# Kernel optimization log

Measured on AMD Instinct MI355X. Metric: run time of the kernel, lower is better.

## Reference

```python
import jax, jax.numpy as jnp
import numpy as np

C = 32            # multiplicity per irrep (node irreps = 32x0e + 32x1o)
N_NODES = 50000
N_EDGES = 800000
R_DIM = 8         # radial embedding dim
R_HID = 8         # radial MLP hidden width
N_SPECIES = 5
AVG_NEIGH = 16.0
N_PATHS = 4       # 0ex0e->0e, 0ex1o->1o, 1ox0e->1o, 1ox1o->0e


def setup_inputs() -> dict:
    key = jax.random.key(0)
    ks = jax.random.split(key, 16)
    inp = {
        'node_features': jax.random.normal(ks[0], (N_NODES, 4 * C), jnp.float32),
        'edge_features': jax.random.normal(ks[1], (N_EDGES, 4), jnp.float32),
        'radial_embedding': jax.random.normal(ks[2], (N_EDGES, R_DIM), jnp.float32),
        'senders': jax.random.randint(ks[3], (N_EDGES,), 0, N_NODES),
        'receivers': jax.random.randint(ks[4], (N_EDGES,), 0, N_NODES),
        'node_species': jax.random.randint(ks[5], (N_NODES,), 0, N_SPECIES),
        # linear_up: per-irrep (block-diagonal) mixing
        'W_up_s': jax.random.normal(ks[6], (C, C), jnp.float32),
        'W_up_v': jax.random.normal(ks[7], (C, C), jnp.float32),
        # radial MLP (no biases, e3nn-style): R_DIM -> R_HID -> N_PATHS*C
        'W_r1': jax.random.normal(ks[8], (R_DIM, R_HID), jnp.float32),
        'W_r2': jax.random.normal(ks[9], (R_HID, N_PATHS * C), jnp.float32),
        # linear_down: 2C x 0e -> 2C (C feats + C gates); 2C x 1o -> C x 1o
        'W_down_s': jax.random.normal(ks[10], (2 * C, 2 * C), jnp.float32),
        'W_down_v': jax.random.normal(ks[11], (2 * C, C), jnp.float32),
        # species-indexed skip connection to gate irreps
        'W_skip_s': jax.random.normal(ks[12], (N_SPECIES, C, 2 * C), jnp.float32),
        'W_skip_v': jax.random.normal(ks[13], (N_SPECIES, C, C), jnp.float32),
    }
    return inp


def reference(node_features, edge_features, radial_embedding, senders, receivers,
              node_species, W_up_s, W_up_v, W_r1, W_r2, W_down_s, W_down_v,
              W_skip_s, W_skip_v):
    N = node_features.shape[0]
    inv_sqrt_C = 1.0 / np.sqrt(C)
    # split irreps: scalars [N,C] and vectors [N,C,3]
    s = node_features[:, :C]
    v = node_features[:, C:].reshape(N, C, 3)
    # ---- linear_up (block-diagonal irreps Linear, fan-in normalized) ----
    s_up = (s @ W_up_s) * inv_sqrt_C
    v_up = jnp.einsum('ncx,cd->ndx', v, W_up_v) * inv_sqrt_C
    # ---- radial MLP -> per-edge tensor-product path weights ----
    h = jax.nn.silu((radial_embedding @ W_r1) * (1.0 / np.sqrt(R_DIM)))
    w = ((h @ W_r2) * (1.0 / np.sqrt(R_HID))).reshape(-1, N_PATHS, C)  # [E,4,C]
    # ---- tensor product messages over edges ----
    sh0 = edge_features[:, 0]      # [E]  l=0
    sh1 = edge_features[:, 1:4]    # [E,3] l=1
    se = s_up[senders]             # [E,C]
    ve = v_up[senders]             # [E,C,3]
    m0 = jnp.concatenate([
        w[:, 0] * se * sh0[:, None],                                      # 0e x 0e -> 0e
        w[:, 3] * jnp.einsum('ecx,ex->ec', ve, sh1) * (1.0 / np.sqrt(3.0))  # 1o x 1o -> 0e
    ], axis=1)                                                            # [E,2C]
    m1 = jnp.concatenate([
        w[:, 1, :, None] * se[:, :, None] * sh1[:, None, :],              # 0e x 1o -> 1o
        w[:, 2, :, None] * ve * sh0[:, None, None],                       # 1o x 0e -> 1o
    ], axis=1)                                                            # [E,2C,3]
    # ---- scatter aggregate to receivers, normalize by sqrt(avg neigh) ----
    inv_sqrt_deg = 1.0 / np.sqrt(AVG_NEIGH)
    agg0 = jax.ops.segment_sum(m0, receivers, num_segments=N) * inv_sqrt_deg
    agg1 = jax.ops.segment_sum(m1, receivers, num_segments=N) * inv_sqrt_deg
    # ---- linear_down to gate irreps (2C x 0e: C feats + C gates; C x 1o) ----
    inv_sqrt_2C = 1.0 / np.sqrt(2 * C)
    sc = (agg0 @ W_down_s) * inv_sqrt_2C                     # [N,2C]
    vc = jnp.einsum('ncx,cd->ndx', agg1, W_down_v) * inv_sqrt_2C  # [N,C,3]
    # ---- species-indexed skip connection ----
    skip_s = jnp.einsum('nc,ncd->nd', s, W_skip_s[node_species]) * inv_sqrt_C
    skip_v = jnp.einsum('ncx,ncd->ndx', v, W_skip_v[node_species]) * inv_sqrt_C
    sc = 0.5 * (sc + skip_s)
    vc = 0.5 * (vc + skip_v)
    # ---- gated nonlinearity: silu on scalars, silu(gates) * vectors ----
    feats = jax.nn.silu(sc[:, :C])
    gates = jax.nn.silu(sc[:, C:])
    vg = vc * gates[:, :, None]
    return jnp.concatenate([feats, vg.reshape(N, 3 * C)], axis=1)  # [N,4C]
```

## Files before the change

### kernel.cpp

```cpp
#include <hip/hip_runtime.h>
#include <stdint.h>

__device__ __forceinline__ float b2f(unsigned short u) {
    union { uint32_t i; float f; } v; v.i = ((uint32_t)u) << 16; return v.f;
}
__device__ __forceinline__ unsigned short f2b(float f) {
    union { float f; uint32_t i; } v; v.f = f;
    uint32_t i = v.i;
    uint32_t r = (i + 0x7fffu + ((i >> 16) & 1u)) >> 16;
    return (unsigned short)r;
}
__device__ __forceinline__ float silu_f(float x) { return x / (1.f + __expf(-x)); }

template<bool BF>
__device__ __forceinline__ float ldin(const void* p, size_t i) {
    if (BF) return b2f(((const unsigned short*)p)[i]);
    return ((const float*)p)[i];
}
template<bool BF>
__device__ __forceinline__ void ld4(const void* p, size_t i, float o[4]) {
    if (BF) {
        const ushort4 u = *(const ushort4*)((const unsigned short*)p + i);
        o[0] = b2f(u.x); o[1] = b2f(u.y); o[2] = b2f(u.z); o[3] = b2f(u.w);
    } else {
        const float4 f = *(const float4*)((const float*)p + i);
        o[0] = f.x; o[1] = f.y; o[2] = f.z; o[3] = f.w;
    }
}
template<bool BF>
__device__ __forceinline__ void stout(void* p, size_t i, float v) {
    if (BF) ((unsigned short*)p)[i] = f2b(v);
    else    ((float*)p)[i] = v;
}

#define INV_SQRT_C   0.17677669529663687f
#define INV_SQRT_8   0.3535533905932738f
#define INV_SQRT_3   0.5773502691896258f
#define INV_SQRT_DEG 0.25f
#define INV_SQRT_2C  0.125f

__device__ __forceinline__ bool detect_bf(const void* nf) {
    const int lane = threadIdx.x & 63;
    const uint32_t w = ((const uint32_t*)nf)[lane];
    const uint32_t ex = (w >> 7) & 0xFFu;
    const unsigned long long m = __ballot(ex >= 96u && ex <= 130u);
    return __popcll(m) > 32;
}

template<bool BF>
__device__ __forceinline__ void prep_phase(
    const void* __restrict__ nf, const void* __restrict__ Wus,
    const void* __restrict__ Wuv, const void* __restrict__ radial,
    const void* __restrict__ ef, const int* __restrict__ senders,
    const int* __restrict__ recv, const void* __restrict__ Wr1,
    unsigned short* __restrict__ stage, uint4* __restrict__ epack,
    int* __restrict__ counts, int* __restrict__ table,
    int* __restrict__ ovcnt, int* __restrict__ ovlist, int N, int E)
{
    const int tid = threadIdx.x;
    __shared__ float sin_[256];
    const int half = tid >> 7;
    const int t = tid & 127;
    const int npairs = (N + 1) >> 1;
    for (int pair = blockIdx.x; pair < npairs; pair += gridDim.x) {
        const int n = pair * 2 + half;
        __syncthreads();
        if (n < N) sin_[half * 128 + t] = ldin<BF>(nf, (size_t)n * 128 + t);
        __syncthreads();
        if (n < N) {
            const float* sb = &sin_[half * 128];
            float acc = 0.f;
            if (t < 32) {
                #pragma unroll 8
                for (int c = 0; c < 32; ++c) acc += sb[c] * ldin<BF>(Wus, c * 32 + t);
                stage[(size_t)n * 128 + t] = f2b(acc * INV_SQRT_C);
            } else {
                const int q = t - 32;
                const int x = q >> 5;
                const int d = q & 31;
                #pragma unroll 8
                for (int c = 0; c < 32; ++c) acc += sb[32 + c * 3 + x] * ldin<BF>(Wuv, c * 32 + d);
                stage[(size_t)n * 128 + 32 + x * 32 + d] = f2b(acc * INV_SQRT_C);
            }
        }
    }
    for (int base = blockIdx.x * 256; base < E; base += gridDim.x * 256) {
        const int e = base + tid;
        if (e >= E) continue;
        float r[8];
        ld4<BF>(radial, (size_t)e * 8, r);
        ld4<BF>(radial, (size_t)e * 8 + 4, r + 4);
        unsigned short h[8];
        #pragma unroll
        for (int j = 0; j < 8; ++j) {
            float pre = 0.f;
            #pragma unroll
            for (int k = 0; k < 8; ++k) pre += r[k] * ldin<BF>(Wr1, k * 8 + j);
            pre *= INV_SQRT_8;
            h[j] = f2b(silu_f(pre) * INV_SQRT_8);
        }
        uint32_t ef01, ef23;
        if (BF) {
            const uint2 tv = *(const uint2*)((const unsigned short*)ef + (size_t)e * 4);
            ef01 = tv.x; ef23 = tv.y;
        } else {
            const float4 fv = *(const float4*)((const float*)ef + (size_t)e * 4);
            ef01 = (uint32_t)f2b(fv.x) | ((uint32_t)f2b(fv.y) << 16);
            ef23 = (uint32_t)f2b(fv.z) | ((uint32_t)f2b(fv.w) << 16);
        }
        const uint32_t snd = (uint32_t)senders[e];
        uint4 a, b;
        a.x = snd; a.y = ef01; a.z = ef23;
        a.w = (uint32_t)h[0] | ((uint32_t)h[1] << 16);
        b.x = (uint32_t)h[2] | ((uint32_t)h[3] << 16);
        b.y = (uint32_t)h[4] | ((uint32_t)h[5] << 16);
        b.z = (uint32_t)h[6] | ((uint32_t)h[7] << 16);
        b.w = 0;
        epack[(size_t)e * 2]     = a;
        epack[(size_t)e * 2 + 1] = b;
        const int rr = recv[e];
        const int pos = atomicAdd(&counts[rr], 1);
        if (pos < 64) table[(size_t)rr * 64 + pos] = e;
        else          ovlist[atomicAdd(ovcnt, 1)] = e;
    }
}
__global__ __launch_bounds__(256) void k_prep(
    const void* nf, const void* Wus, const void* Wuv, const void* radial,
    const void* ef, const int* senders, const int* recv, const void* Wr1,
    unsigned short* stage, uint4* epack,
    int* counts, int* table, int* ovlist, int N, int E)
{
    int* ovcnt = counts + N;
    if (detect_bf(nf)) prep_phase<true >(nf, Wus, Wuv, radial, ef, senders, recv, Wr1,
                                         stage, epack, counts, table, ovcnt, ovlist, N, E);
    else               prep_phase<false>(nf, Wus, Wuv, radial, ef, senders, recv, Wr1,
                                         stage, epack, counts, table, ovcnt, ovlist, N, E);
}

#define STAGE_LOAD(k, B0, B1, B2) do { \
    const int sk_ = __shfl(snd_r, (k), 64); \
    const unsigned short* rec_ = stage + (size_t)sk_ * 128; \
    if (lane < 32) { B0 = rec_[lane]; } \
    else { B0 = rec_[32 + d]; B1 = rec_[64 + d]; B2 = rec_[96 + d]; } \
} while (0)

#define EDGE_BODY(i, B0, B1, B2) do { \
    const uint32_t a_ = (uint32_t)__shfl((int)ef0, (i), 64); \
    const uint32_t bb_ = (uint32_t)__shfl((int)ef1, (i), 64); \
    const float sh0 = b2f((unsigned short)(a_ & 0xFFFFu)); \
    const float s1x = b2f((unsigned short)(a_ >> 16)); \
    const float s1y = b2f((unsigned short)(bb_ & 0xFFFFu)); \
    const float s1z = b2f((unsigned short)(bb_ >> 16)); \
    const uint32_t ua = (uint32_t)__shfl((int)h0, (i), 64); \
    const uint32_t ub = (uint32_t)__shfl((int)h1, (i), 64); \
    const uint32_t uc = (uint32_t)__shfl((int)h2, (i), 64); \
    const uint32_t ud = (uint32_t)__shfl((int)h3, (i), 64); \
    float hh[8]; \
    hh[0] = b2f((unsigned short)(ua & 0xFFFFu)); hh[1] = b2f((unsigned short)(ua >> 16)); \
    hh[2] = b2f((unsigned short)(ub & 0xFFFFu)); hh[3] = b2f((unsigned short)(ub >> 16)); \
    hh[4] = b2f((unsigned short)(uc & 0xFFFFu)); hh[5] = b2f((unsigned short)(uc >> 16)); \
    hh[6] = b2f((unsigned short)(ud & 0xFFFFu)); hh[7] = b2f((unsigned short)(ud >> 16)); \
    const float vA = hh[0]*wA[0]+hh[1]*wA[1]+hh[2]*wA[2]+hh[3]*wA[3] \
                   + hh[4]*wA[4]+hh[5]*wA[5]+hh[6]*wA[6]+hh[7]*wA[7]; \
    const float vB = hh[0]*wB[0]+hh[1]*wB[1]+hh[2]*wB[2]+hh[3]*wB[3] \
                   + hh[4]*wB[4]+hh[5]*wB[5]+hh[6]*wB[6]+hh[7]*wB[7]; \
    if (lane < 32) { \
        const float se = b2f((unsigned short)(B0)); \
        acc0 += vA * se * sh0; \
        const float tt = vB * se; \
        a1x += tt * s1x; a1y += tt * s1y; a1z += tt * s1z; \
    } else { \
        const float vx = b2f((unsigned short)(B0)); \
        const float vy = b2f((unsigned short)(B1)); \
        const float vz = b2f((unsigned short)(B2)); \
        acc0 += vB * (vx * s1x + vy * s1y + vz * s1z) * INV_SQRT_3; \
        const float tt = vA * sh0; \
        a1x += tt * vx; a1y += tt * vy; a1z += tt * vz; \
    } \
} while (0)

template<bool BF>
__device__ __forceinline__ void agg_body(
    const void* __restrict__ nf, const int* __restrict__ recv,
    const int* __restrict__ species,
    const void* __restrict__ Wr2, const void* __restrict__ Wds,
    const void* __restrict__ Wdv, const void* __restrict__ Wss,
    const void* __restrict__ Wsv,
    const unsigned short* __restrict__ stage,
    const uint4* __restrict__ epack,
    const int* __restrict__ counts, const int* __restrict__ table,
    const int* __restrict__ ovcnt, const int* __restrict__ ovlist,
    void* __restrict__ out, int N)
{
    __shared__ float lds_agg0[4][64];
    __shared__ float lds_agg1[4][3][65];
    __shared__ float lds_scf[4][64];
    const int wave = threadIdx.x >> 6;
    const int lane = threadIdx.x & 63;
    const int n = blockIdx.x * 4 + wave;
    const bool valid = (n < N);
    int sp = 0;

    if (valid) {
        sp = species[n];
        const int cnt = counts[n];
        const int colA = (lane < 32) ? lane : lane + 32;
        float wA[8], wB[8];
        #pragma unroll
        for (int j = 0; j < 8; ++j) {
            wA[j] = ldin<BF>(Wr2, j * 128 + colA);
            wB[j] = ldin<BF>(Wr2, j * 128 + colA + 32);
        }

        const int mc = (cnt < 64) ? cnt : 64;
        int snd_r = 0;
        uint32_t ef0 = 0, ef1 = 0, h0 = 0, h1 = 0, h2 = 0, h3 = 0;
        if (lane < mc) {
            const int eid = table[(size_t)n * 64 + lane];
            const uint4 a = epack[(size_t)eid * 2];
            const uint4 b = epack[(size_t)eid * 2 + 1];
            snd_r = (int)a.x; ef0 = a.y; ef1 = a.z;
            h0 = a.w; h1 = b.x; h2 = b.y; h3 = b.z;
        }

        float acc0 = 0.f, a1x = 0.f, a1y = 0.f, a1z = 0.f;
        const int d = lane - 32;
        const int mcp = (mc + 3) & ~3;

        uint32_t c0a=0,c1a=0,c2a=0, c0b=0,c1b=0,c2b=0,
                 c0c=0,c1c=0,c2c=0, c0d=0,c1d=0,c2d=0;
        if (mcp > 0) {
            STAGE_LOAD(0, c0a, c1a, c2a);
            if (1 < mcp) STAGE_LOAD(1, c0b, c1b, c2b);
            if (2 < mcp) STAGE_LOAD(2, c0c, c1c, c2c);
            for (int i = 0; i + 4 <= mcp; i += 4) {
                STAGE_LOAD(i + 3, c0d, c1d, c2d);
                EDGE_BODY(i, c0a, c1a, c2a);
                if (i + 4 < mcp) STAGE_LOAD(i + 4, c0a, c1a, c2a);
                EDGE_BODY(i + 1, c0b, c1b, c2b);
                if (i + 5 < mcp) STAGE_LOAD(i + 5, c0b, c1b, c2b);
                EDGE_BODY(i + 2, c0c, c1c, c2c);
                if (i + 6 < mcp) STAGE_LOAD(i + 6, c0c, c1c, c2c);
                EDGE_BODY(i + 3, c0d, c1d, c2d);
            }
        }
        if (cnt > 64) {
            const int oc = *ovcnt;
            for (int i2 = 0; i2 < oc; ++i2) {
                const int e = ovlist[i2];
                if (recv[e] != n) continue;
                const uint4 a = epack[(size_t)e * 2];
                const uint4 b = epack[(size_t)e * 2 + 1];
                const float sh0 = b2f((unsigned short)(a.y & 0xFFFFu));
                const float s1x = b2f((unsigned short)(a.y >> 16));
                const float s1y = b2f((unsigned short)(a.z & 0xFFFFu));
                const float s1z = b2f((unsigned short)(a.z >> 16));
                float hh[8];
                hh[0] = b2f((unsigned short)(a.w & 0xFFFFu)); hh[1] = b2f((unsigned short)(a.w >> 16));
                hh[2] = b2f((unsigned short)(b.x & 0xFFFFu)); hh[3] = b2f((unsigned short)(b.x >> 16));
                hh[4] = b2f((unsigned short)(b.y & 0xFFFFu)); hh[5] = b2f((unsigned short)(b.y >> 16));
                hh[6] = b2f((unsigned short)(b.z & 0xFFFFu)); hh[7] = b2f((unsigned short)(b.z >> 16));
                const float vA = hh[0]*wA[0]+hh[1]*wA[1]+hh[2]*wA[2]+hh[3]*wA[3]
                               + hh[4]*wA[4]+hh[5]*wA[5]+hh[6]*wA[6]+hh[7]*wA[7];
                const float vB = hh[0]*wB[0]+hh[1]*wB[1]+hh[2]*wB[2]+hh[3]*wB[3]
                               + hh[4]*wB[4]+hh[5]*wB[5]+hh[6]*wB[6]+hh[7]*wB[7];
                const unsigned short* rec = stage + (size_t)a.x * 128;
                if (lane < 32) {
                    const float se = b2f(rec[lane]);
                    acc0 += vA * se * sh0;
                    const float tt = vB * se;
                    a1x += tt * s1x; a1y += tt * s1y; a1z += tt * s1z;
                } else {
                    const float vx = b2f(rec[32 + d]), vy = b2f(rec[64 + d]), vz = b2f(rec[96 + d]);
                    acc0 += vB * (vx * s1x + vy * s1y + vz * s1z) * INV_SQRT_3;
                    const float tt = vA * sh0;
                    a1x += tt * vx; a1y += tt * vy; a1z += tt * vz;
                }
            }
        }
        lds_agg0[wave][lane]    = acc0 * INV_SQRT_DEG;
        lds_agg1[wave][0][lane] = a1x * INV_SQRT_DEG;
        lds_agg1[wave][1][lane] = a1y * INV_SQRT_DEG;
        lds_agg1[wave][2][lane] = a1z * INV_SQRT_DEG;
    }
    __syncthreads();
    if (valid) {
        float sc = 0.f;
        #pragma unroll 8
        for (int c = 0; c < 64; ++c) sc += lds_agg0[wave][c] * ldin<BF>(Wds, c * 64 + lane);
        sc *= INV_SQRT_2C;
        float ss = 0.f;
        #pragma unroll 8
        for (int c = 0; c < 32; ++c)
            ss += ldin<BF>(nf, (size_t)n * 128 + c) * ldin<BF>(Wss, (size_t)sp * 2048 + c * 64 + lane);
        ss *= INV_SQRT_C;
        lds_scf[wave][lane] = 0.5f * (sc + ss);
    }
    __syncthreads();
    if (valid) {
        #pragma unroll
        for (int rr = 0; rr < 2; ++rr) {
            const int p = lane + rr * 64;
            float outv;
            if (p < 32) {
                outv = silu_f(lds_scf[wave][p]);
            } else {
                const int o = p - 32;
                const int c = o / 3;
                const int x = o - 3 * c;
                float vc = 0.f;
                #pragma unroll 8
                for (int c2 = 0; c2 < 64; ++c2) vc += lds_agg1[wave][x][c2] * ldin<BF>(Wdv, c2 * 32 + c);
                vc *= INV_SQRT_2C;
                float sv = 0.f;
                #pragma unroll 8
                for (int c2 = 0; c2 < 32; ++c2)
                    sv += ldin<BF>(nf, (size_t)n * 128 + 32 + c2 * 3 + x) * ldin<BF>(Wsv, (size_t)sp * 1024 + c2 * 32 + c);
                sv *= INV_SQRT_C;
                const float g2 = silu_f(lds_scf[wave][32 + c]);
                outv = 0.5f * (vc + sv) * g2;
            }
            stout<BF>(out, (size_t)n * 128 + p, outv);
        }
    }
}
__global__ __launch_bounds__(256) void k_aggregate(
    const void* nf, const int* recv, const int* species,
    const void* Wr2, const void* Wds, const void* Wdv, const void* Wss, const void* Wsv,
    const unsigned short* stage, const uint4* epack,
    const int* counts, const int* table, const int* ovlist, void* out, int N)
{
    const int* ovcnt = counts + N;
    if (detect_bf(nf)) agg_body<true >(nf, recv, species, Wr2, Wds, Wdv, Wss, Wsv,
                                       stage, epack, counts, table, ovcnt, ovlist, out, N);
    else               agg_body<false>(nf, recv, species, Wr2, Wds, Wdv, Wss, Wsv,
                                       stage, epack, counts, table, ovcnt, ovlist, out, N);
}

extern "C" void kernel_launch(void* const* d_in, const int* in_sizes, int n_in,
                              void* d_out, int out_size, void* d_ws, size_t ws_size,
                              hipStream_t stream) {
    const void* nf      = d_in[0];
    const void* ef      = d_in[1];
    const void* radial  = d_in[2];
    const int*  senders = (const int*)d_in[3];
    const int*  recv    = (const int*)d_in[4];
    const int*  specie  = (const int*)d_in[5];
    const void* Wus = d_in[6];
    const void* Wuv = d_in[7];
    const void* Wr1 = d_in[8];
    const void* Wr2 = d_in[9];
    const void* Wds = d_in[10];
    const void* Wdv = d_in[11];
    const void* Wss = d_in[12];
    const void* Wsv = d_in[13];

    const int N = in_sizes[5];
    const int E = in_sizes[3];

    const size_t stageB = (size_t)N * 128 * 2;
    const size_t epackB = (size_t)E * 32;
    const size_t tableB = (size_t)N * 64 * 4;
    const size_t need   = stageB + epackB + tableB + (size_t)(N + 1 + E) * 4;
    if (ws_size < need) return;

    char* ws = (char*)d_ws;
    unsigned short* stage = (unsigned short*)ws;
    uint4* epack = (uint4*)(ws + stageB);
    int* table   = (int*)(ws + stageB + epackB);
    int* counts  = (int*)(ws + stageB + epackB + tableB);
    int* ovlist  = counts + N + 1;

    hipMemsetAsync(counts, 0, (size_t)(N + 1) * sizeof(int), stream);
    k_prep<<<2048, 256, 0, stream>>>(nf, Wus, Wuv, radial, ef, senders, recv, Wr1,
                                     stage, epack, counts, table, ovlist, N, E);
    k_aggregate<<<(N + 3) / 4, 256, 0, stream>>>(nf, recv, specie,
                                                 Wr2, Wds, Wdv, Wss, Wsv,
                                                 stage, epack, counts, table, ovlist,
                                                 d_out, N);
}
```

Baseline: 450.4 us.

## Split each node's edge aggregation across four waves with LDS reduction

The aggregate kernel now assigns one node per 256-thread block instead of one node per wave. Each wave handles a 16-edge segment of the node's edge table, and the partial sums are reduced through shared memory before the down-projection and gating, which run on one or two waves. This shortens the serial per-wave edge loop and raises memory-level parallelism on the gathers. In exchange it launches four times as many blocks, adds two barriers and LDS traffic, and leaves most threads idle during the epilogue.

```diff
diff --git a/kernel.cpp b/kernel.cpp
--- a/kernel.cpp
+++ b/kernel.cpp
@@ -192,136 +192,136 @@
     const int* __restrict__ ovcnt, const int* __restrict__ ovlist,
     void* __restrict__ out, int N)
 {
-    __shared__ float lds_agg0[4][64];
-    __shared__ float lds_agg1[4][3][65];
-    __shared__ float lds_scf[4][64];
-    const int wave = threadIdx.x >> 6;
-    const int lane = threadIdx.x & 63;
-    const int n = blockIdx.x * 4 + wave;
-    const bool valid = (n < N);
-    int sp = 0;
-
-    if (valid) {
-        sp = species[n];
-        const int cnt = counts[n];
-        const int colA = (lane < 32) ? lane : lane + 32;
-        float wA[8], wB[8];
-        #pragma unroll
-        for (int j = 0; j < 8; ++j) {
-            wA[j] = ldin<BF>(Wr2, j * 128 + colA);
-            wB[j] = ldin<BF>(Wr2, j * 128 + colA + 32);
-        }
-
-        const int mc = (cnt < 64) ? cnt : 64;
-        int snd_r = 0;
-        uint32_t ef0 = 0, ef1 = 0, h0 = 0, h1 = 0, h2 = 0, h3 = 0;
-        if (lane < mc) {
-            const int eid = table[(size_t)n * 64 + lane];
-            const uint4 a = epack[(size_t)eid * 2];
-            const uint4 b = epack[(size_t)eid * 2 + 1];
-            snd_r = (int)a.x; ef0 = a.y; ef1 = a.z;
-            h0 = a.w; h1 = b.x; h2 = b.y; h3 = b.z;
-        }
-
-        float acc0 = 0.f, a1x = 0.f, a1y = 0.f, a1z = 0.f;
-        const int d = lane - 32;
-        const int mcp = (mc + 3) & ~3;
-
-        uint32_t c0a=0,c1a=0,c2a=0, c0b=0,c1b=0,c2b=0,
-                 c0c=0,c1c=0,c2c=0, c0d=0,c1d=0,c2d=0;
-        if (mcp > 0) {
-            STAGE_LOAD(0, c0a, c1a, c2a);
-            if (1 < mcp) STAGE_LOAD(1, c0b, c1b, c2b);
-            if (2 < mcp) STAGE_LOAD(2, c0c, c1c, c2c);
-            for (int i = 0; i + 4 <= mcp; i += 4) {
-                STAGE_LOAD(i + 3, c0d, c1d, c2d);
-                EDGE_BODY(i, c0a, c1a, c2a);
-                if (i + 4 < mcp) STAGE_LOAD(i + 4, c0a, c1a, c2a);
-                EDGE_BODY(i + 1, c0b, c1b, c2b);
-                if (i + 5 < mcp) STAGE_LOAD(i + 5, c0b, c1b, c2b);
-                EDGE_BODY(i + 2, c0c, c1c, c2c);
-                if (i + 6 < mcp) STAGE_LOAD(i + 6, c0c, c1c, c2c);
-                EDGE_BODY(i + 3, c0d, c1d, c2d);
+    __shared__ float lds_p[4][4][64];
+    __shared__ float red[4][66];
+    __shared__ float lds_scf[64];
+    const int tid = threadIdx.x;
+    const int wave = tid >> 6;
+    const int lane = tid & 63;
+    const int n = blockIdx.x;
+
+    const int sp = species[n];
+    const int cnt = counts[n];
+    const int mc = (cnt < 64) ? cnt : 64;
+    const int seg = wave * 16;
+    int len = mc - seg; if (len < 0) len = 0; if (len > 16) len = 16;
+
+    const int colA = (lane < 32) ? lane : lane + 32;
+    float wA[8], wB[8];
+    #pragma unroll
+    for (int j = 0; j < 8; ++j) {
+        wA[j] = ldin<BF>(Wr2, j * 128 + colA);
+        wB[j] = ldin<BF>(Wr2, j * 128 + colA + 32);
+    }
+
+    int snd_r = 0;
+    uint32_t ef0 = 0, ef1 = 0, h0 = 0, h1 = 0, h2 = 0, h3 = 0;
+    if (lane < len) {
+        const int eid = table[(size_t)n * 64 + seg + lane];
+        const uint4 a = epack[(size_t)eid * 2];
+        const uint4 b = epack[(size_t)eid * 2 + 1];
+        snd_r = (int)a.x; ef0 = a.y; ef1 = a.z;
+        h0 = a.w; h1 = b.x; h2 = b.y; h3 = b.z;
+    }
+
+    float acc0 = 0.f, a1x = 0.f, a1y = 0.f, a1z = 0.f;
+    const int d = lane - 32;
+    const int mcp = (len + 3) & ~3;
+
+    uint32_t c0a=0,c1a=0,c2a=0, c0b=0,c1b=0,c2b=0,
+             c0c=0,c1c=0,c2c=0, c0d=0,c1d=0,c2d=0;
+    if (mcp > 0) {
+        STAGE_LOAD(0, c0a, c1a, c2a);
+        if (1 < mcp) STAGE_LOAD(1, c0b, c1b, c2b);
+        if (2 < mcp) STAGE_LOAD(2, c0c, c1c, c2c);
+        for (int i = 0; i + 4 <= mcp; i += 4) {
+            STAGE_LOAD(i + 3, c0d, c1d, c2d);
+            EDGE_BODY(i, c0a, c1a, c2a);
+            if (i + 4 < mcp) STAGE_LOAD(i + 4, c0a, c1a, c2a);
+            EDGE_BODY(i + 1, c0b, c1b, c2b);
+            if (i + 5 < mcp) STAGE_LOAD(i + 5, c0b, c1b, c2b);
+            EDGE_BODY(i + 2, c0c, c1c, c2c);
+            if (i + 6 < mcp) STAGE_LOAD(i + 6, c0c, c1c, c2c);
+            EDGE_BODY(i + 3, c0d, c1d, c2d);
+        }
+    }
+    if (wave == 0 && cnt > 64) {
+        const int oc = *ovcnt;
+        for (int i2 = 0; i2 < oc; ++i2) {
+            const int e = ovlist[i2];
+            if (recv[e] != n) continue;
+            const uint4 a = epack[(size_t)e * 2];
+            const uint4 b = epack[(size_t)e * 2 + 1];
+            const float sh0 = b2f((unsigned short)(a.y & 0xFFFFu));
+            const float s1x = b2f((unsigned short)(a.y >> 16));
+            const float s1y = b2f((unsigned short)(a.z & 0xFFFFu));
+            const float s1z = b2f((unsigned short)(a.z >> 16));
+            float hh[8];
+            hh[0] = b2f((unsigned short)(a.w & 0xFFFFu)); hh[1] = b2f((unsigned short)(a.w >> 16));
+            hh[2] = b2f((unsigned short)(b.x & 0xFFFFu)); hh[3] = b2f((unsigned short)(b.x >> 16));
+            hh[4] = b2f((unsigned short)(b.y & 0xFFFFu)); hh[5] = b2f((unsigned short)(b.y >> 16));
+            hh[6] = b2f((unsigned short)(b.z & 0xFFFFu)); hh[7] = b2f((unsigned short)(b.z >> 16));
+            const float vA = hh[0]*wA[0]+hh[1]*wA[1]+hh[2]*wA[2]+hh[3]*wA[3]
+                           + hh[4]*wA[4]+hh[5]*wA[5]+hh[6]*wA[6]+hh[7]*wA[7];
+            const float vB = hh[0]*wB[0]+hh[1]*wB[1]+hh[2]*wB[2]+hh[3]*wB[3]
+                           + hh[4]*wB[4]+hh[5]*wB[5]+hh[6]*wB[6]+hh[7]*wB[7];
+            const unsigned short* rec = stage + (size_t)a.x * 128;
+            if (lane < 32) {
+                const float se = b2f(rec[lane]);
+                acc0 += vA * se * sh0;
+                const float tt = vB * se;
+                a1x += tt * s1x; a1y += tt * s1y; a1z += tt * s1z;
+            } else {
+                const float vx = b2f(rec[32 + d]), vy = b2f(rec[64 + d]), vz = b2f(rec[96 + d]);
+                acc0 += vB * (vx * s1x + vy * s1y + vz * s1z) * INV_SQRT_3;
+                const float tt = vA * sh0;
+                a1x += tt * vx; a1y += tt * vy; a1z += tt * vz;
             }
         }
-        if (cnt > 64) {
-            const int oc = *ovcnt;
-            for (int i2 = 0; i2 < oc; ++i2) {
-                const int e = ovlist[i2];
-                if (recv[e] != n) continue;
-                const uint4 a = epack[(size_t)e * 2];
-                const uint4 b = epack[(size_t)e * 2 + 1];
-                const float sh0 = b2f((unsigned short)(a.y & 0xFFFFu));
-                const float s1x = b2f((unsigned short)(a.y >> 16));
-                const float s1y = b2f((unsigned short)(a.z & 0xFFFFu));
-                const float s1z = b2f((unsigned short)(a.z >> 16));
-                float hh[8];
-                hh[0] = b2f((unsigned short)(a.w & 0xFFFFu)); hh[1] = b2f((unsigned short)(a.w >> 16));
-                hh[2] = b2f((unsigned short)(b.x & 0xFFFFu)); hh[3] = b2f((unsigned short)(b.x >> 16));
-                hh[4] = b2f((unsigned short)(b.y & 0xFFFFu)); hh[5] = b2f((unsigned short)(b.y >> 16));
-                hh[6] = b2f((unsigned short)(b.z & 0xFFFFu)); hh[7] = b2f((unsigned short)(b.z >> 16));
-                const float vA = hh[0]*wA[0]+hh[1]*wA[1]+hh[2]*wA[2]+hh[3]*wA[3]
-                               + hh[4]*wA[4]+hh[5]*wA[5]+hh[6]*wA[6]+hh[7]*wA[7];
-                const float vB = hh[0]*wB[0]+hh[1]*wB[1]+hh[2]*wB[2]+hh[3]*wB[3]
-                               + hh[4]*wB[4]+hh[5]*wB[5]+hh[6]*wB[6]+hh[7]*wB[7];
-                const unsigned short* rec = stage + (size_t)a.x * 128;
-                if (lane < 32) {
-                    const float se = b2f(rec[lane]);
-                    acc0 += vA * se * sh0;
-                    const float tt = vB * se;
-                    a1x += tt * s1x; a1y += tt * s1y; a1z += tt * s1z;
-                } else {
-                    const float vx = b2f(rec[32 + d]), vy = b2f(rec[64 + d]), vz = b2f(rec[96 + d]);
-                    acc0 += vB * (vx * s1x + vy * s1y + vz * s1z) * INV_SQRT_3;
-                    const float tt = vA * sh0;
-                    a1x += tt * vx; a1y += tt * vy; a1z += tt * vz;
-                }
-            }
-        }
-        lds_agg0[wave][lane]    = acc0 * INV_SQRT_DEG;
-        lds_agg1[wave][0][lane] = a1x * INV_SQRT_DEG;
-        lds_agg1[wave][1][lane] = a1y * INV_SQRT_DEG;
-        lds_agg1[wave][2][lane] = a1z * INV_SQRT_DEG;
-    }
+    }
+    lds_p[wave][0][lane] = acc0;
+    lds_p[wave][1][lane] = a1x;
+    lds_p[wave][2][lane] = a1y;
+    lds_p[wave][3][lane] = a1z;
     __syncthreads();
-    if (valid) {
+    red[wave][lane] = (lds_p[0][wave][lane] + lds_p[1][wave][lane]
+                     + lds_p[2][wave][lane] + lds_p[3][wave][lane]) * INV_SQRT_DEG;
+    __syncthreads();
+    if (tid < 64) {
         float sc = 0.f;
         #pragma unroll 8
-        for (int c = 0; c < 64; ++c) sc += lds_agg0[wave][c] * ldin<BF>(Wds, c * 64 + lane);
+        for (int c = 0; c < 64; ++c) sc += red[0][c] * ldin<BF>(Wds, c * 64 + tid);
         sc *= INV_SQRT_2C;
         float ss = 0.f;
         #pragma unroll 8
         for (int c = 0; c < 32; ++c)
-            ss += ldin<BF>(nf, (size_t)n * 128 + c) * ldin<BF>(Wss, (size_t)sp * 2048 + c * 64 + lane);
+            ss += ldin<BF>(nf, (size_t)n * 128 + c) * ldin<BF>(Wss, (size_t)sp * 2048 + c * 64 + tid);
         ss *= INV_SQRT_C;
-        lds_scf[wave][lane] = 0.5f * (sc + ss);
+        lds_scf[tid] = 0.5f * (sc + ss);
     }
     __syncthreads();
-    if (valid) {
-        #pragma unroll
-        for (int rr = 0; rr < 2; ++rr) {
-            const int p = lane + rr * 64;
-            float outv;
-            if (p < 32) {
-                outv = silu_f(lds_scf[wave][p]);
-            } else {
-                const int o = p - 32;
-                const int c = o / 3;
-                const int x = o - 3 * c;
-                float vc = 0.f;
-                #pragma unroll 8
-                for (int c2 = 0; c2 < 64; ++c2) vc += lds_agg1[wave][x][c2] * ldin<BF>(Wdv, c2 * 32 + c);
-                vc *= INV_SQRT_2C;
-                float sv = 0.f;
-                #pragma unroll 8
-                for (int c2 = 0; c2 < 32; ++c2)
-                    sv += ldin<BF>(nf, (size_t)n * 128 + 32 + c2 * 3 + x) * ldin<BF>(Wsv, (size_t)sp * 1024 + c2 * 32 + c);
-                sv *= INV_SQRT_C;
-                const float g2 = silu_f(lds_scf[wave][32 + c]);
-                outv = 0.5f * (vc + sv) * g2;
-            }
-            stout<BF>(out, (size_t)n * 128 + p, outv);
-        }
+    if (tid < 128) {
+        const int p = tid;
+        float outv;
+        if (p < 32) {
+            outv = silu_f(lds_scf[p]);
+        } else {
+            const int o = p - 32;
+            const int c = o / 3;
+            const int x = o - 3 * c;
+            float vc = 0.f;
+            #pragma unroll 8
+            for (int c2 = 0; c2 < 64; ++c2) vc += red[1 + x][c2] * ldin<BF>(Wdv, c2 * 32 + c);
+            vc *= INV_SQRT_2C;
+            float sv = 0.f;
+            #pragma unroll 8
+            for (int c2 = 0; c2 < 32; ++c2)
+                sv += ldin<BF>(nf, (size_t)n * 128 + 32 + c2 * 3 + x) * ldin<BF>(Wsv, (size_t)sp * 1024 + c2 * 32 + c);
+            sv *= INV_SQRT_C;
+            const float g2 = silu_f(lds_scf[32 + c]);
+            outv = 0.5f * (vc + sv) * g2;
+        }
+        stout<BF>(out, (size_t)n * 128 + p, outv);
     }
 }
 __global__ __launch_bounds__(256) void k_aggregate(
@@ -374,8 +374,8 @@
     hipMemsetAsync(counts, 0, (size_t)(N + 1) * sizeof(int), stream);
     k_prep<<<2048, 256, 0, stream>>>(nf, Wus, Wuv, radial, ef, senders, recv, Wr1,
                                      stage, epack, counts, table, ovlist, N, E);
-    k_aggregate<<<(N + 3) / 4, 256, 0, stream>>>(nf, recv, specie,
-                                                 Wr2, Wds, Wdv, Wss, Wsv,
-                                                 stage, epack, counts, table, ovlist,
-                                                 d_out, N);
-}
+    k_aggregate<<<N, 256, 0, stream>>>(nf, recv, specie,
+                                       Wr2, Wds, Wdv, Wss, Wsv,
+                                       stage, epack, counts, table, ovlist,
+                                       d_out, N);
+}
```

New measurement: 639.6 us. +42.0%, slower.

## Write packed edge records directly into per-receiver slot table

Applied to the files above, without the earlier changes.

The prep kernel now scatters each edge's 32-byte packed record straight into a per-receiver slot array (32 slots) instead of writing an edge-indexed epack plus a 64-slot table of edge ids. The aggregate kernel then reads its records contiguously per node and drops the extra level of indirection through the table. Overflow edges beyond 32 per receiver are recomputed from the raw inputs (radial MLP, edge features, sender) in a slow linear scan of the overflow list. That path runs rarely for an average degree of 16, but it costs more for high-degree nodes.

```diff
diff --git a/kernel.cpp b/kernel.cpp
--- a/kernel.cpp
+++ b/kernel.cpp
@@ -38,6 +38,7 @@
 #define INV_SQRT_3   0.5773502691896258f
 #define INV_SQRT_DEG 0.25f
 #define INV_SQRT_2C  0.125f
+#define SLOTS 32
 
 __device__ __forceinline__ bool detect_bf(const void* nf) {
     const int lane = threadIdx.x & 63;
@@ -53,9 +54,9 @@
     const void* __restrict__ Wuv, const void* __restrict__ radial,
     const void* __restrict__ ef, const int* __restrict__ senders,
     const int* __restrict__ recv, const void* __restrict__ Wr1,
-    unsigned short* __restrict__ stage, uint4* __restrict__ epack,
-    int* __restrict__ counts, int* __restrict__ table,
-    int* __restrict__ ovcnt, int* __restrict__ ovlist, int N, int E)
+    unsigned short* __restrict__ stage, uint4* __restrict__ trec,
+    int* __restrict__ counts, int* __restrict__ ovcnt, int* __restrict__ ovlist,
+    int N, int E)
 {
     const int tid = threadIdx.x;
     __shared__ float sin_[256];
@@ -108,33 +109,33 @@
             ef01 = (uint32_t)f2b(fv.x) | ((uint32_t)f2b(fv.y) << 16);
             ef23 = (uint32_t)f2b(fv.z) | ((uint32_t)f2b(fv.w) << 16);
         }
-        const uint32_t snd = (uint32_t)senders[e];
         uint4 a, b;
-        a.x = snd; a.y = ef01; a.z = ef23;
+        a.x = (uint32_t)senders[e]; a.y = ef01; a.z = ef23;
         a.w = (uint32_t)h[0] | ((uint32_t)h[1] << 16);
         b.x = (uint32_t)h[2] | ((uint32_t)h[3] << 16);
         b.y = (uint32_t)h[4] | ((uint32_t)h[5] << 16);
         b.z = (uint32_t)h[6] | ((uint32_t)h[7] << 16);
         b.w = 0;
-        epack[(size_t)e * 2]     = a;
-        epack[(size_t)e * 2 + 1] = b;
         const int rr = recv[e];
         const int pos = atomicAdd(&counts[rr], 1);
-        if (pos < 64) table[(size_t)rr * 64 + pos] = e;
-        else          ovlist[atomicAdd(ovcnt, 1)] = e;
+        if (pos < SLOTS) {
+            trec[((size_t)rr * SLOTS + pos) * 2]     = a;
+            trec[((size_t)rr * SLOTS + pos) * 2 + 1] = b;
+        } else {
+            ovlist[atomicAdd(ovcnt, 1)] = e;
+        }
     }
 }
 __global__ __launch_bounds__(256) void k_prep(
     const void* nf, const void* Wus, const void* Wuv, const void* radial,
     const void* ef, const int* senders, const int* recv, const void* Wr1,
-    unsigned short* stage, uint4* epack,
-    int* counts, int* table, int* ovlist, int N, int E)
+    unsigned short* stage, uint4* trec, int* counts, int* ovlist, int N, int E)
 {
     int* ovcnt = counts + N;
     if (detect_bf(nf)) prep_phase<true >(nf, Wus, Wuv, radial, ef, senders, recv, Wr1,
-                                         stage, epack, counts, table, ovcnt, ovlist, N, E);
+                                         stage, trec, counts, ovcnt, ovlist, N, E);
     else               prep_phase<false>(nf, Wus, Wuv, radial, ef, senders, recv, Wr1,
-                                         stage, epack, counts, table, ovcnt, ovlist, N, E);
+                                         stage, trec, counts, ovcnt, ovlist, N, E);
 }
 
 #define STAGE_LOAD(k, B0, B1, B2) do { \
@@ -181,16 +182,15 @@
 
 template<bool BF>
 __device__ __forceinline__ void agg_body(
-    const void* __restrict__ nf, const int* __restrict__ recv,
-    const int* __restrict__ species,
-    const void* __restrict__ Wr2, const void* __restrict__ Wds,
-    const void* __restrict__ Wdv, const void* __restrict__ Wss,
-    const void* __restrict__ Wsv,
-    const unsigned short* __restrict__ stage,
-    const uint4* __restrict__ epack,
-    const int* __restrict__ counts, const int* __restrict__ table,
-    const int* __restrict__ ovcnt, const int* __restrict__ ovlist,
-    void* __restrict__ out, int N)
+    const void* __restrict__ nf, const void* __restrict__ radial,
+    const void* __restrict__ ef, const int* __restrict__ senders,
+    const int* __restrict__ recv, const int* __restrict__ species,
+    const void* __restrict__ Wr1, const void* __restrict__ Wr2,
+    const void* __restrict__ Wds, const void* __restrict__ Wdv,
+    const void* __restrict__ Wss, const void* __restrict__ Wsv,
+    const unsigned short* __restrict__ stage, const uint4* __restrict__ trec,
+    const int* __restrict__ counts, const int* __restrict__ ovcnt,
+    const int* __restrict__ ovlist, void* __restrict__ out, int N)
 {
     __shared__ float lds_agg0[4][64];
     __shared__ float lds_agg1[4][3][65];
@@ -212,13 +212,12 @@
             wB[j] = ldin<BF>(Wr2, j * 128 + colA + 32);
         }
 
-        const int mc = (cnt < 64) ? cnt : 64;
+        const int mc = (cnt < SLOTS) ? cnt : SLOTS;
         int snd_r = 0;
         uint32_t ef0 = 0, ef1 = 0, h0 = 0, h1 = 0, h2 = 0, h3 = 0;
         if (lane < mc) {
-            const int eid = table[(size_t)n * 64 + lane];
-            const uint4 a = epack[(size_t)eid * 2];
-            const uint4 b = epack[(size_t)eid * 2 + 1];
+            const uint4 a = trec[((size_t)n * SLOTS + lane) * 2];
+            const uint4 b = trec[((size_t)n * SLOTS + lane) * 2 + 1];
             snd_r = (int)a.x; ef0 = a.y; ef1 = a.z;
             h0 = a.w; h1 = b.x; h2 = b.y; h3 = b.z;
         }
@@ -244,27 +243,31 @@
                 EDGE_BODY(i + 3, c0d, c1d, c2d);
             }
         }
-        if (cnt > 64) {
+        if (cnt > SLOTS) {
             const int oc = *ovcnt;
             for (int i2 = 0; i2 < oc; ++i2) {
                 const int e = ovlist[i2];
                 if (recv[e] != n) continue;
-                const uint4 a = epack[(size_t)e * 2];
-                const uint4 b = epack[(size_t)e * 2 + 1];
-                const float sh0 = b2f((unsigned short)(a.y & 0xFFFFu));
-                const float s1x = b2f((unsigned short)(a.y >> 16));
-                const float s1y = b2f((unsigned short)(a.z & 0xFFFFu));
-                const float s1z = b2f((unsigned short)(a.z >> 16));
+                float r[8];
+                ld4<BF>(radial, (size_t)e * 8, r);
+                ld4<BF>(radial, (size_t)e * 8 + 4, r + 4);
                 float hh[8];
-                hh[0] = b2f((unsigned short)(a.w & 0xFFFFu)); hh[1] = b2f((unsigned short)(a.w >> 16));
-                hh[2] = b2f((unsigned short)(b.x & 0xFFFFu)); hh[3] = b2f((unsigned short)(b.x >> 16));
-                hh[4] = b2f((unsigned short)(b.y & 0xFFFFu)); hh[5] = b2f((unsigned short)(b.y >> 16));
-                hh[6] = b2f((unsigned short)(b.z & 0xFFFFu)); hh[7] = b2f((unsigned short)(b.z >> 16));
+                #pragma unroll
+                for (int j = 0; j < 8; ++j) {
+                    float pre = 0.f;
+                    #pragma unroll
+                    for (int k = 0; k < 8; ++k) pre += r[k] * ldin<BF>(Wr1, k * 8 + j);
+                    pre *= INV_SQRT_8;
+                    hh[j] = b2f(f2b(silu_f(pre) * INV_SQRT_8));
+                }
+                float efv[4];
+                ld4<BF>(ef, (size_t)e * 4, efv);
+                const float sh0 = efv[0], s1x = efv[1], s1y = efv[2], s1z = efv[3];
                 const float vA = hh[0]*wA[0]+hh[1]*wA[1]+hh[2]*wA[2]+hh[3]*wA[3]
                                + hh[4]*wA[4]+hh[5]*wA[5]+hh[6]*wA[6]+hh[7]*wA[7];
                 const float vB = hh[0]*wB[0]+hh[1]*wB[1]+hh[2]*wB[2]+hh[3]*wB[3]
                                + hh[4]*wB[4]+hh[5]*wB[5]+hh[6]*wB[6]+hh[7]*wB[7];
-                const unsigned short* rec = stage + (size_t)a.x * 128;
+                const unsigned short* rec = stage + (size_t)senders[e] * 128;
                 if (lane < 32) {
                     const float se = b2f(rec[lane]);
                     acc0 += vA * se * sh0;
@@ -325,16 +328,20 @@
     }
 }
 __global__ __launch_bounds__(256) void k_aggregate(
-    const void* nf, const int* recv, const int* species,
-    const void* Wr2, const void* Wds, const void* Wdv, const void* Wss, const void* Wsv,
-    const unsigned short* stage, const uint4* epack,
-    const int* counts, const int* table, const int* ovlist, void* out, int N)
+    const void* nf, const void* radial, const void* ef,
+    const int* senders, const int* recv, const int* species,
+    const void* Wr1, const void* Wr2, const void* Wds, const void* Wdv,
+    const void* Wss, const void* Wsv,
+    const unsigned short* stage, const uint4* trec,
+    const int* counts, const int* ovlist, void* out, int N)
 {
     const int* ovcnt = counts + N;
-    if (detect_bf(nf)) agg_body<true >(nf, recv, species, Wr2, Wds, Wdv, Wss, Wsv,
-                                       stage, epack, counts, table, ovcnt, ovlist, out, N);
-    else               agg_body<false>(nf, recv, species, Wr2, Wds, Wdv, Wss, Wsv,
-                                       stage, epack, counts, table, ovcnt, ovlist, out, N);
+    if (detect_bf(nf)) agg_body<true >(nf, radial, ef, senders, recv, species,
+                                       Wr1, Wr2, Wds, Wdv, Wss, Wsv,
+                                       stage, trec, counts, ovcnt, ovlist, out, N);
+    else               agg_body<false>(nf, radial, ef, senders, recv, species,
+                                       Wr1, Wr2, Wds, Wdv, Wss, Wsv,
+                                       stage, trec, counts, ovcnt, ovlist, out, N);
 }
 
 extern "C" void kernel_launch(void* const* d_in, const int* in_sizes, int n_in,
@@ -359,23 +366,21 @@
     const int E = in_sizes[3];
 
     const size_t stageB = (size_t)N * 128 * 2;
-    const size_t epackB = (size_t)E * 32;
-    const size_t tableB = (size_t)N * 64 * 4;
-    const size_t need   = stageB + epackB + tableB + (size_t)(N + 1 + E) * 4;
+    const size_t trecB  = (size_t)N * SLOTS * 32;
+    const size_t need   = stageB + trecB + (size_t)(N + 1 + E) * 4;
     if (ws_size < need) return;
 
     char* ws = (char*)d_ws;
     unsigned short* stage = (unsigned short*)ws;
-    uint4* epack = (uint4*)(ws + stageB);
-    int* table   = (int*)(ws + stageB + epackB);
-    int* counts  = (int*)(ws + stageB + epackB + tableB);
+    uint4* trec  = (uint4*)(ws + stageB);
+    int* counts  = (int*)(ws + stageB + trecB);
     int* ovlist  = counts + N + 1;
 
     hipMemsetAsync(counts, 0, (size_t)(N + 1) * sizeof(int), stream);
     k_prep<<<2048, 256, 0, stream>>>(nf, Wus, Wuv, radial, ef, senders, recv, Wr1,
-                                     stage, epack, counts, table, ovlist, N, E);
-    k_aggregate<<<(N + 3) / 4, 256, 0, stream>>>(nf, recv, specie,
-                                                 Wr2, Wds, Wdv, Wss, Wsv,
-                                                 stage, epack, counts, table, ovlist,
+                                     stage, trec, counts, ovlist, N, E);
+    k_aggregate<<<(N + 3) / 4, 256, 0, stream>>>(nf, radial, ef, senders, recv, specie,
+                                                 Wr1, Wr2, Wds, Wdv, Wss, Wsv,
+                                                 stage, trec, counts, ovlist,
                                                  d_out, N);
 }
```

New measurement: 467.7 us. +3.8%, slower.
